# Kernel tuning notes

Hardware: AMD Instinct MI355X
Metric: run time of the kernel (lower is better)

The kernel has to match this reference:

```python
import jax, jax.numpy as jnp
import numpy as np

N = 100000   # nodes
E = 1600000  # edges
IN = 3       # in_channels
H = 32       # hidden_channels
C = 10       # num_classes_dynamic (== num output classes here)
G = 64       # number of graphs in the batch


def setup_inputs() -> dict:
    key = jax.random.key(0)
    ks = jax.random.split(key, 12)
    def w(k, shape, fan_in):
        return jax.random.normal(k, shape, jnp.float32) / np.sqrt(fan_in).astype(np.float32)
    inp = {}
    inp["x"] = jax.random.normal(ks[0], (N, IN), jnp.float32)
    inp["edge_index"] = jax.random.randint(ks[1], (2, E), 0, N, jnp.int32)
    inp["batch"] = jnp.sort(jax.random.randint(ks[2], (N,), 0, G, jnp.int32))
    # per-class linear filters (DynamicEdgeConv.filters)
    inp["filt_W"] = w(ks[3], (C, IN, H), IN)
    inp["filt_b"] = jnp.zeros((C, H), jnp.float32)
    # shared edge MLP: Linear(2H,H) -> ReLU -> Linear(H,H)
    inp["mlp_W1"] = w(ks[4], (2 * H, H), 2 * H)
    inp["mlp_b1"] = jnp.zeros((H,), jnp.float32)
    inp["mlp_W2"] = w(ks[5], (H, H), H)
    inp["mlp_b2"] = jnp.zeros((H,), jnp.float32)
    # GCN layers (gcn1 input dim hardcoded 323 = IN + C*H)
    inp["gcn1_W"] = w(ks[6], (IN + C * H, H), IN + C * H)
    inp["gcn1_b"] = jnp.zeros((H,), jnp.float32)
    inp["gcn2_W"] = w(ks[7], (H, H), H)
    inp["gcn2_b"] = jnp.zeros((H,), jnp.float32)
    # classifier
    inp["cls_W"] = w(ks[8], (H, C), H)
    inp["cls_b"] = jnp.zeros((C,), jnp.float32)
    return inp


def _gcn_conv(x, W, b, row, col, dinv):
    # PyG GCNConv: add self-loops, sym-normalize, aggregate src->dst
    xw = x @ W                                   # [N, H]
    norm = dinv[row] * dinv[col]                 # [E]
    out = jax.ops.segment_sum(xw[row] * norm[:, None], col, num_segments=x.shape[0])
    out = out + xw * (dinv * dinv)[:, None]      # self-loop term, norm = 1/deg_i
    return out + b


def _forward(x, edge_index, batch, filt_W, filt_b, mlp_W1, mlp_b1, mlp_W2, mlp_b2,
             gcn1_W, gcn1_b, gcn2_W, gcn2_b, cls_W, cls_b):
    row, col = edge_index[0], edge_index[1]
    n = x.shape[0]

    # DynamicEdgeConv: per-class filter -> gather(row,col) -> edge MLP -> scatter_add into col
    def per_class(_, wb):
        Wc, bc = wb
        xc = x @ Wc + bc                                      # [N, H]
        ef = jnp.concatenate([xc[row], xc[col]], axis=1)      # [E, 2H]
        h = jax.nn.relu(ef @ mlp_W1 + mlp_b1) @ mlp_W2 + mlp_b2
        return None, jax.ops.segment_sum(h, col, num_segments=n)
    _, aggs = jax.lax.scan(per_class, None, (filt_W, filt_b))  # [C, N, H]

    feat = jnp.concatenate([x, aggs.transpose(1, 0, 2).reshape(n, -1)], axis=1)  # [N, IN + C*H]

    deg = jax.ops.segment_sum(jnp.ones(row.shape[0], x.dtype), col, num_segments=n) + 1.0
    dinv = deg ** -0.5
    h1 = jax.nn.relu(_gcn_conv(feat, gcn1_W, gcn1_b, row, col, dinv))
    h2 = jax.nn.relu(_gcn_conv(h1, gcn2_W, gcn2_b, row, col, dinv))

    counts = jax.ops.segment_sum(jnp.ones(n, x.dtype), batch, num_segments=G)
    pooled = jax.ops.segment_sum(h2, batch, num_segments=G) / jnp.maximum(counts, 1.0)[:, None]
    return pooled @ cls_W + cls_b                             # [G, C]


def reference(x, edge_index, batch, filt_W, filt_b, mlp_W1, mlp_b1, mlp_W2, mlp_b2,
              gcn1_W, gcn1_b, gcn2_W, gcn2_b, cls_W, cls_b):
    return _forward(x, edge_index, batch, filt_W, filt_b, mlp_W1, mlp_b1, mlp_W2, mlp_b2,
                    gcn1_W, gcn1_b, gcn2_W, gcn2_b, cls_W, cls_b)
```

## Files before the change

### kernel.cpp

```cpp
#include <hip/hip_runtime.h>

#define NN 100000
#define NE 1600000
#define HH 32
#define CC 10
#define GG 64
#define NB 391
#define PBLK 100
#define ECH 16000
#define MTOT (NB * PBLK)
#define MSB ((MTOT + 255) / 256)

typedef _Float16 half8 __attribute__((ext_vector_type(8)));
typedef _Float16 half2v __attribute__((ext_vector_type(2)));
typedef float f32x4 __attribute__((ext_vector_type(4)));

__device__ __forceinline__ half2v bch(int v) { return __builtin_bit_cast(half2v, v); }


__global__ void precompute_small(const float* __restrict__ fW, const float* __restrict__ fb,
                                 const float* __restrict__ W1, const float* __restrict__ b1,
                                 const float* __restrict__ W2, const float* __restrict__ b2,
                                 const float* __restrict__ g1W, float* __restrict__ tab,
                                 _Float16* __restrict__ Mfrag) {
    int c = blockIdx.x;
    int k = threadIdx.x >> 5;
    int j = threadIdx.x & 31;
    float m = 0.f;
    for (int mm = 0; mm < 32; ++mm)
        m += W2[k * 32 + mm] * g1W[(3 + 32 * c + mm) * 32 + j];
    tab[2240 + c * 1024 + k * 32 + j] = m;

    if (k < 3) {
        float a = 0.f, b = 0.f;
        for (int i = 0; i < 32; ++i) {
            float w = fW[c * 96 + k * 32 + i];
            a += w * W1[i * 32 + j];
            b += w * W1[(32 + i) * 32 + j];
        }
        tab[c * 96 + k * 32 + j] = a;
        tab[960 + c * 96 + k * 32 + j] = b;
    } else if (k == 3) {
        float h = b1[j];
        for (int i = 0; i < 32; ++i)
            h += fb[c * 32 + i] * (W1[i * 32 + j] + W1[(32 + i) * 32 + j]);
        tab[1920 + c * 32 + j] = h;
    } else if (k == 4 && c == 0) {
        float t = 0.f;
        for (int cc2 = 0; cc2 < CC; ++cc2)
            for (int mm = 0; mm < 32; ++mm)
                t += b2[mm] * g1W[(3 + 32 * cc2 + mm) * 32 + j];
        tab[12480 + j] = t;
    }
    __syncthreads();
    {
        int jch = k;
        int jcol = j;
        float v = tab[2240 + c * 1024 + jch * 32 + jcol];
        int knew = (c >> 1) * 64 + 2 * jch + (c & 1);
        int kc = knew >> 5, within = knew & 31;
        int jt = jcol >> 4;
        int lq = within >> 3, ii = within & 7;
        int lidx = lq * 16 + (jcol & 15);
        int flat = ((kc * 2 + jt) * 64 + lidx) * 8 + ii;
        Mfrag[flat] = (_Float16)v;
    }
}

__global__ void bucket_hist(const int* __restrict__ ei, int* __restrict__ mat) {
    __shared__ int h[NB];
    int blk = blockIdx.x, tid = threadIdx.x;
    for (int i = tid; i < NB; i += 256) h[i] = 0;
    __syncthreads();
    int base = blk * ECH;
    for (int k = tid; k < ECH; k += 256)
        atomicAdd(&h[ei[NE + base + k] >> 8], 1);
    __syncthreads();
    for (int i = tid; i < NB; i += 256) mat[i * PBLK + blk] = h[i];
}

__global__ void scan_m1(const int* __restrict__ mat, int* __restrict__ msum) {
    __shared__ int sh[256];
    int b = blockIdx.x, t = threadIdx.x;
    int i = b * 256 + t;
    sh[t] = (i < MTOT) ? mat[i] : 0;
    __syncthreads();
    for (int off = 128; off > 0; off >>= 1) {
        if (t < off) sh[t] += sh[t + off];
        __syncthreads();
    }
    if (t == 0) msum[b] = sh[0];
}

__global__ void scan_m2(int* __restrict__ msum, float* __restrict__ pooled) {
    for (int i = threadIdx.x; i < GG * 33; i += 256) pooled[i] = 0.0f;
    __shared__ int sh[256];
    int t = threadIdx.x;
    int v = (t < MSB) ? msum[t] : 0;
    sh[t] = v;
    __syncthreads();
    for (int off = 1; off < 256; off <<= 1) {
        int add = (t >= off) ? sh[t - off] : 0;
        __syncthreads();
        sh[t] += add;
        __syncthreads();
    }
    if (t < MSB) msum[t] = sh[t] - v;
}

__global__ void scan_m3(int* __restrict__ mat, const int* __restrict__ msum) {
    __shared__ int sh[256];
    int b = blockIdx.x, t = threadIdx.x;
    int i = b * 256 + t;
    int v = (i < MTOT) ? mat[i] : 0;
    sh[t] = v;
    __syncthreads();
    for (int off = 1; off < 256; off <<= 1) {
        int add = (t >= off) ? sh[t - off] : 0;
        __syncthreads();
        sh[t] += add;
        __syncthreads();
    }
    if (i < MTOT) mat[i] = sh[t] - v + msum[b];
}

__global__ void bucket_scatter(const int* __restrict__ ei, const int* __restrict__ mat,
                               unsigned int* __restrict__ part) {
    __shared__ int bas[NB];
    __shared__ int cur[NB];
    int blk = blockIdx.x, tid = threadIdx.x;
    for (int i = tid; i < NB; i += 256) { bas[i] = mat[i * PBLK + blk]; cur[i] = 0; }
    __syncthreads();
    int base = blk * ECH;
    for (int k = tid; k < ECH; k += 256) {
        int e = base + k;
        int r = ei[e];
        int c = ei[NE + e];
        int b = c >> 8;
        int local = atomicAdd(&cur[b], 1);
        part[bas[b] + local] = (unsigned)r | ((unsigned)(c & 255) << 24);
    }
}

__global__ void bucket_build(const unsigned int* __restrict__ part, const int* __restrict__ mat,
                             const float* __restrict__ x, int* __restrict__ csr_row,
                             int* __restrict__ ideg, int* __restrict__ offs,
                             float* __restrict__ dinv, float4* __restrict__ xpad,
                             uint4* __restrict__ xs) {
    __shared__ int lh[256];
    __shared__ int lex[256];
    __shared__ int cur[256];
    int b = blockIdx.x, tid = threadIdx.x;
    int ebase = mat[b * PBLK];
    int eend = (b == NB - 1) ? NE : mat[(b + 1) * PBLK];
    int m = eend - ebase;
    lh[tid] = 0;
    __syncthreads();
    for (int k = tid; k < m; k += 256) {
        unsigned v = part[ebase + k];
        atomicAdd(&lh[v >> 24], 1);
    }
    __syncthreads();
    int cnt = lh[tid];
    lex[tid] = cnt;
    __syncthreads();
    for (int off = 1; off < 256; off <<= 1) {
        int v = (tid >= off) ? lex[tid - off] : 0;
        __syncthreads();
        lex[tid] += v;
        __syncthreads();
    }
    int excl = lex[tid] - cnt;
    lex[tid] = excl;
    cur[tid] = 0;
    int n = b * 256 + tid;
    if (n < NN) {
        ideg[n] = cnt;
        offs[n] = ebase + excl;
        float di = rsqrtf((float)cnt + 1.0f);
        dinv[n] = di;
        float x0 = x[n * 3], x1 = x[n * 3 + 1], x2 = x[n * 3 + 2];
        xpad[n] = make_float4(x0, x1, x2, di);
        _Float16 hx = (_Float16)x0, hy = (_Float16)x1, hz = (_Float16)x2;
        half2v sx = {hx, hx}, sy = {hy, hy}, sz = {hz, hz};
        xs[n] = make_uint4(__builtin_bit_cast(unsigned int, sx),
                           __builtin_bit_cast(unsigned int, sy),
                           __builtin_bit_cast(unsigned int, sz), 0u);
    }
    if (b == 0 && tid == 0) offs[NN] = NE;
    __syncthreads();
    for (int k = tid; k < m; k += 256) {
        unsigned v = part[ebase + k];
        int cl = (int)(v >> 24);
        int r = (int)(v & 0x00FFFFFFu);
        int local = atomicAdd(&cur[cl], 1);
        csr_row[ebase + lex[cl] + local] = r;
    }
}

#define EC_PAIR(QQ, SRC) do { \
    half2v px_ = bch(__shfl((int)(QQ).x, (SRC), 64)); \
    half2v py_ = bch(__shfl((int)(QQ).y, (SRC), 64)); \
    half2v pz_ = bch(__shfl((int)(QQ).z, (SRC), 64)); \
    _Pragma("unroll") \
    for (int p = 0; p < 5; ++p) { \
        half2v v = va[p] + px_ * A0[p] + py_ * A1[p] + pz_ * A2[p]; \
        v = __builtin_elementwise_max(v, zero); \
        acc[p] += v; \
    } } while (0)

#define EC_FLUSH() do { \
    _Pragma("unroll") \
    for (int p = 0; p < 5; ++p) { \
        accf[2 * p]     += (float)acc[p].x; \
        accf[2 * p + 1] += (float)acc[p].y; \
        acc[p] = zero; \
    } } while (0)

#define EC_GROUP4(QQ, TB) do { \
    half2v gx_[4], gy_[4], gz_[4]; \
    _Pragma("unroll") \
    for (int u = 0; u < 4; ++u) { \
        int s_ = 2 * ((TB) + u) + half; \
        gx_[u] = bch(__shfl((int)(QQ).x, s_, 64)); \
        gy_[u] = bch(__shfl((int)(QQ).y, s_, 64)); \
        gz_[u] = bch(__shfl((int)(QQ).z, s_, 64)); \
    } \
    _Pragma("unroll") \
    for (int u = 0; u < 4; ++u) { \
        _Pragma("unroll") \
        for (int p = 0; p < 5; ++p) { \
            half2v v = va[p] + gx_[u] * A0[p] + gy_[u] * A1[p] + gz_[u] * A2[p]; \
            v = __builtin_elementwise_max(v, zero); \
            acc[p] += v; \
        } \
    } \
    EC_FLUSH(); } while (0)

#define EC_CHUNK_FROM(T0, QQ, C2) do { \
    int tfull_ = (C2) >> 1; \
    int t_ = (T0); \
    for (; t_ + 4 <= tfull_; t_ += 4) EC_GROUP4(QQ, t_); \
    for (; t_ < tfull_; ++t_) EC_PAIR(QQ, 2 * t_ + half); \
    if ((C2) & 1) { \
        int src_ = (C2) - 1; \
        half2v px_ = bch(__shfl((int)(QQ).x, src_, 64)); \
        half2v py_ = bch(__shfl((int)(QQ).y, src_, 64)); \
        half2v pz_ = bch(__shfl((int)(QQ).z, src_, 64)); \
        if (half == 0) { \
            _Pragma("unroll") \
            for (int p = 0; p < 5; ++p) { \
                half2v v = va[p] + px_ * A0[p] + py_ * A1[p] + pz_ * A2[p]; \
                v = __builtin_elementwise_max(v, zero); \
                acc[p] += v; \
            } \
        } \
    } \
    EC_FLUSH(); } while (0)

__global__ __launch_bounds__(256, 4) void edgeconv_fused(
    const uint4* __restrict__ xs, const int* __restrict__ offs,
    const int* __restrict__ csr_row, const float* __restrict__ tab,
    _Float16* __restrict__ aggh) {
    int lane = threadIdx.x & 63;
    int j = lane & 31;
    int half = lane >> 5;

    half2v A0[5], A1[5], A2[5], B0[5], B1[5], B2[5], hb[5];
#pragma unroll
    for (int p = 0; p < 5; ++p) {
        int c0 = 2 * p, c1 = 2 * p + 1;
        A0[p] = half2v{(_Float16)tab[c0 * 96 + j],        (_Float16)tab[c1 * 96 + j]};
        A1[p] = half2v{(_Float16)tab[c0 * 96 + 32 + j],   (_Float16)tab[c1 * 96 + 32 + j]};
        A2[p] = half2v{(_Float16)tab[c0 * 96 + 64 + j],   (_Float16)tab[c1 * 96 + 64 + j]};
        B0[p] = half2v{(_Float16)tab[960 + c0 * 96 + j],      (_Float16)tab[960 + c1 * 96 + j]};
        B1[p] = half2v{(_Float16)tab[960 + c0 * 96 + 32 + j], (_Float16)tab[960 + c1 * 96 + 32 + j]};
        B2[p] = half2v{(_Float16)tab[960 + c0 * 96 + 64 + j], (_Float16)tab[960 + c1 * 96 + 64 + j]};
        hb[p] = half2v{(_Float16)tab[1920 + c0 * 32 + j], (_Float16)tab[1920 + c1 * 32 + j]};
    }
    const half2v zero = half2v{(_Float16)0.f, (_Float16)0.f};

    int wid = blockIdx.x * 4 + (threadIdx.x >> 6);
    const int ws = gridDim.x * 4;

    int n = wid;
    if (n >= NN) return;
    int e0 = offs[n];
    int e1 = offs[n + 1];
    uint4 qn = xs[n];
    int n2 = n + ws;
    int e0n = 0, e1n = 0;
    if (n2 < NN) { e0n = offs[n2]; e1n = offs[n2 + 1]; }
    uint4 q;
    {
        int ee = e0 + lane;
        int r0 = (ee < e1) ? csr_row[ee] : 0;
        q = xs[r0];
    }

    while (true) {
        int n3 = n2 + ws;
        int e0n2 = 0, e1n2 = 0;
        if (n3 < NN) { e0n2 = offs[n3]; e1n2 = offs[n3 + 1]; }
        uint4 qn2 = make_uint4(0u, 0u, 0u, 0u);
        if (n2 < NN) qn2 = xs[n2];

        bool multi = (e1 - e0) > 64;
        int pb = multi ? (e0 + 64) : e0n;
        int pe = multi ? e1 : e1n;
        int ee2 = pb + lane;
        int rn = (ee2 < pe) ? csr_row[ee2] : 0;

        half2v pxn = bch((int)qn.x), pyn = bch((int)qn.y), pzn = bch((int)qn.z);
        half2v va[5], acc[5];
        float accf[10];
#pragma unroll
        for (int p = 0; p < 5; ++p) {
            va[p] = hb[p] + pxn * B0[p] + pyn * B1[p] + pzn * B2[p];
            acc[p] = zero;
            accf[2 * p] = 0.f;
            accf[2 * p + 1] = 0.f;
        }

        int c2 = e1 - e0;
        if (c2 > 64) c2 = 64;
        int t0 = 0;
        if ((c2 >> 1) >= 4) {
            EC_GROUP4(q, 0);
            t0 = 4;
        }
        uint4 qpre = xs[rn];
        EC_CHUNK_FROM(t0, q, c2);

        if (multi) {
            int base = e0 + 64;
            uint4 qc = qpre;
            while (true) {
                int cc = e1 - base;
                if (cc > 64) cc = 64;
                int nb = base + 64;
                bool m2 = nb < e1;
                int pb2 = m2 ? nb : e0n;
                int pe2 = m2 ? e1 : e1n;
                int ee3 = pb2 + lane;
                int rn2 = (ee3 < pe2) ? csr_row[ee3] : 0;
                uint4 qp2 = xs[rn2];
                EC_CHUNK_FROM(0, qc, cc);
                qc = qp2;
                if (!m2) break;
                base = nb;
            }
            qpre = qc;
        }

#pragma unroll
        for (int c = 0; c < 10; ++c) accf[c] += __shfl_xor(accf[c], 32, 64);
        unsigned* arow32 = (unsigned*)(aggh + (size_t)n * 320);
        half2v d0 = {(_Float16)accf[2 * half],     (_Float16)accf[2 * half + 1]};
        half2v d1 = {(_Float16)accf[4 + 2 * half], (_Float16)accf[4 + 2 * half + 1]};
        arow32[lane]      = __builtin_bit_cast(unsigned, d0);
        arow32[64 + lane] = __builtin_bit_cast(unsigned, d1);
        if (half == 0) {
            half2v d2 = {(_Float16)accf[8], (_Float16)accf[9]};
            arow32[128 + lane] = __builtin_bit_cast(unsigned, d2);
        }

        if (n2 >= NN) return;
        n = n2;
        n2 = n3;
        e0 = e0n; e1 = e1n;
        e0n = e0n2; e1n = e1n2;
        qn = qn2;
        q = qpre;
    }
}

__global__ __launch_bounds__(256) void fold_mfma(
    const _Float16* __restrict__ aggh, const _Float16* __restrict__ MfragG,
    const float4* __restrict__ xpad, const int* __restrict__ ideg,
    const float* __restrict__ tab, const float* __restrict__ g1W,
    _Float16* __restrict__ y1) {
    __shared__ _Float16 Mf[10240];
    {
        const uint4* src = (const uint4*)MfragG;
        uint4* dst = (uint4*)Mf;
        for (int i = threadIdx.x; i < 1280; i += 256) dst[i] = src[i];
    }
    __syncthreads();

    int wave = blockIdx.x * 4 + (threadIdx.x >> 6);
    int lane = threadIdx.x & 63;
    int n0 = wave * 16;
    if (n0 >= NN) return;

    int m = lane & 15, q = lane >> 4;
    int arow_n = n0 + m;
    bool rowok = arow_n < NN;
    const _Float16* arow = aggh + (size_t)arow_n * 320 + q * 8;

    const half8* mf = (const half8*)Mf;
    f32x4 acc0 = {0.f, 0.f, 0.f, 0.f};
    f32x4 acc1 = {0.f, 0.f, 0.f, 0.f};

    for (int kc = 0; kc < 10; ++kc) {
        half8 a;
        if (rowok) a = *(const half8*)(arow + kc * 32);
        else {
#pragma unroll
            for (int i = 0; i < 8; ++i) a[i] = (_Float16)0.f;
        }
        half8 b0 = mf[(kc * 2 + 0) * 64 + lane];
        half8 b1 = mf[(kc * 2 + 1) * 64 + lane];
        acc0 = __builtin_amdgcn_mfma_f32_16x16x32_f16(a, b0, acc0, 0, 0, 0);
        acc1 = __builtin_amdgcn_mfma_f32_16x16x32_f16(a, b1, acc1, 0, 0, 0);
    }

    int jcol = lane & 15;
    float t0 = tab[12480 + jcol],      t1 = tab[12480 + 16 + jcol];
    float w00 = g1W[jcol],      w01 = g1W[32 + jcol],      w02 = g1W[64 + jcol];
    float w10 = g1W[16 + jcol], w11 = g1W[48 + jcol],      w12 = g1W[80 + jcol];
#pragma unroll
    for (int r = 0; r < 4; ++r) {
        int node = n0 + q * 4 + r;
        if (node < NN) {
            float4 xn = xpad[node];
            float dg = (float)ideg[node];
            float v0 = dg * t0 + xn.x * w00 + xn.y * w01 + xn.z * w02 + acc0[r];
            float v1 = dg * t1 + xn.x * w10 + xn.y * w11 + xn.z * w12 + acc1[r];
            y1[node * 32 + jcol]      = (_Float16)(v0 * xn.w);
            y1[node * 32 + 16 + jcol] = (_Float16)(v1 * xn.w);
        }
    }
}

__global__ __launch_bounds__(256, 8) void prop1_fused(
    const int* __restrict__ offs, const int* __restrict__ csr_row,
    const unsigned int* __restrict__ y1p, const float* __restrict__ dinv,
    const float* __restrict__ g1b, const float* __restrict__ g2W,
    unsigned int* __restrict__ y2p) {
    __shared__ float g2s[1024];
    for (int i = threadIdx.x; i < 1024; i += 256) g2s[i] = g2W[i];
    __syncthreads();

    int lane = threadIdx.x & 63;
    int l = lane & 15;
    int wid = blockIdx.x * 4 + (threadIdx.x >> 6);
    int n = wid * 4 + (lane >> 4);
    if (n >= NN) return;

    int e0 = offs[n], e1 = offs[n + 1];
    float sAl = 0.f, sAh = 0.f, sBl = 0.f, sBh = 0.f;
    int e = e0;
    if (e + 7 < e1) {
        half2v p0[8];
        {
            int r0[8];
#pragma unroll
            for (int u = 0; u < 8; ++u) r0[u] = csr_row[e + u];
#pragma unroll
            for (int u = 0; u < 8; ++u) p0[u] = __builtin_bit_cast(half2v, y1p[r0[u] * 16 + l]);
        }
        while (true) {
            int e2 = e + 8;
            bool more = (e2 + 7 < e1);
            half2v p1[8];
            if (more) {
                int r1[8];
#pragma unroll
                for (int u = 0; u < 8; ++u) r1[u] = csr_row[e2 + u];
#pragma unroll
                for (int u = 0; u < 8; ++u) p1[u] = __builtin_bit_cast(half2v, y1p[r1[u] * 16 + l]);
            }
#pragma unroll
            for (int u = 0; u < 8; u += 2) {
                sAl += (float)p0[u].x;     sAh += (float)p0[u].y;
                sBl += (float)p0[u + 1].x; sBh += (float)p0[u + 1].y;
            }
            e = e2;
            if (!more) break;
#pragma unroll
            for (int u = 0; u < 8; ++u) p0[u] = p1[u];
        }
    }
    if (e + 3 < e1) {
        int r[4];
#pragma unroll
        for (int u = 0; u < 4; ++u) r[u] = csr_row[e + u];
        half2v p[4];
#pragma unroll
        for (int u = 0; u < 4; ++u) p[u] = __builtin_bit_cast(half2v, y1p[r[u] * 16 + l]);
        sAl += (float)p[0].x + (float)p[2].x; sAh += (float)p[0].y + (float)p[2].y;
        sBl += (float)p[1].x + (float)p[3].x; sBh += (float)p[1].y + (float)p[3].y;
        e += 4;
    }
    if (e + 1 < e1) {
        int r0 = csr_row[e], r1 = csr_row[e + 1];
        half2v p0 = __builtin_bit_cast(half2v, y1p[r0 * 16 + l]);
        half2v p1 = __builtin_bit_cast(half2v, y1p[r1 * 16 + l]);
        sAl += (float)p0.x; sAh += (float)p0.y;
        sBl += (float)p1.x; sBh += (float)p1.y;
        e += 2;
    }
    if (e < e1) {
        int r = csr_row[e];
        half2v p = __builtin_bit_cast(half2v, y1p[r * 16 + l]);
        sAl += (float)p.x; sAh += (float)p.y;
    }
    float di = dinv[n];
    half2v pn = __builtin_bit_cast(half2v, y1p[n * 16 + l]);
    float h1l = di * (sAl + sBl + (float)pn.x);
    float h1h = di * (sAh + sBh + (float)pn.y);
    float hl = fmaxf(h1l + g1b[2 * l], 0.f);
    float hh = fmaxf(h1h + g1b[2 * l + 1], 0.f);

    float al = 0.f, ah = 0.f;
    int base = lane & 48;
#pragma unroll
    for (int m = 0; m < 16; ++m) {
        float xl = __shfl(hl, base + m, 64);
        float xh2 = __shfl(hh, base + m, 64);
        al += xl * g2s[(2 * m) * 32 + 2 * l] + xh2 * g2s[(2 * m + 1) * 32 + 2 * l];
        ah += xl * g2s[(2 * m) * 32 + 2 * l + 1] + xh2 * g2s[(2 * m + 1) * 32 + 2 * l + 1];
    }
    half2v o = {(_Float16)(al * di), (_Float16)(ah * di)};
    y2p[n * 16 + l] = __builtin_bit_cast(unsigned int, o);
}

__global__ __launch_bounds__(256, 8) void prop2_plain(
    const int* __restrict__ offs, const int* __restrict__ csr_row,
    const unsigned int* __restrict__ y2p, const float* __restrict__ dinv,
    unsigned int* __restrict__ outp) {
    int lane = threadIdx.x & 63;
    int l = lane & 15;
    int wid = blockIdx.x * 4 + (threadIdx.x >> 6);
    int n = wid * 4 + (lane >> 4);
    if (n >= NN) return;

    int e0 = offs[n], e1 = offs[n + 1];
    float sAl = 0.f, sAh = 0.f, sBl = 0.f, sBh = 0.f;
    int e = e0;
    if (e + 7 < e1) {
        half2v p0[8];
        {
            int r0[8];
#pragma unroll
            for (int u = 0; u < 8; ++u) r0[u] = csr_row[e + u];
#pragma unroll
            for (int u = 0; u < 8; ++u) p0[u] = __builtin_bit_cast(half2v, y2p[r0[u] * 16 + l]);
        }
        while (true) {
            int e2 = e + 8;
            bool more = (e2 + 7 < e1);
            half2v p1[8];
            if (more) {
                int r1[8];
#pragma unroll
                for (int u = 0; u < 8; ++u) r1[u] = csr_row[e2 + u];
#pragma unroll
                for (int u = 0; u < 8; ++u) p1[u] = __builtin_bit_cast(half2v, y2p[r1[u] * 16 + l]);
            }
#pragma unroll
            for (int u = 0; u < 8; u += 2) {
                sAl += (float)p0[u].x;     sAh += (float)p0[u].y;
                sBl += (float)p0[u + 1].x; sBh += (float)p0[u + 1].y;
            }
            e = e2;
            if (!more) break;
#pragma unroll
            for (int u = 0; u < 8; ++u) p0[u] = p1[u];
        }
    }
    if (e + 3 < e1) {
        int r[4];
#pragma unroll
        for (int u = 0; u < 4; ++u) r[u] = csr_row[e + u];
        half2v p[4];
#pragma unroll
        for (int u = 0; u < 4; ++u) p[u] = __builtin_bit_cast(half2v, y2p[r[u] * 16 + l]);
        sAl += (float)p[0].x + (float)p[2].x; sAh += (float)p[0].y + (float)p[2].y;
        sBl += (float)p[1].x + (float)p[3].x; sBh += (float)p[1].y + (float)p[3].y;
        e += 4;
    }
    if (e + 1 < e1) {
        int r0 = csr_row[e], r1 = csr_row[e + 1];
        half2v p0 = __builtin_bit_cast(half2v, y2p[r0 * 16 + l]);
        half2v p1 = __builtin_bit_cast(half2v, y2p[r1 * 16 + l]);
        sAl += (float)p0.x; sAh += (float)p0.y;
        sBl += (float)p1.x; sBh += (float)p1.y;
        e += 2;
    }
    if (e < e1) {
        int r = csr_row[e];
        half2v p = __builtin_bit_cast(half2v, y2p[r * 16 + l]);
        sAl += (float)p.x; sAh += (float)p.y;
    }
    float di = dinv[n];
    half2v pn = __builtin_bit_cast(half2v, y2p[n * 16 + l]);
    half2v o = {(_Float16)(di * (sAl + sBl + (float)pn.x)),
                (_Float16)(di * (sAh + sBh + (float)pn.y))};
    outp[n * 16 + l] = __builtin_bit_cast(unsigned int, o);
}

__global__ void pool_seg(const _Float16* __restrict__ h2, const float* __restrict__ g2b,
                         const int* __restrict__ batch, float* __restrict__ pooled,
                         float* __restrict__ counts) {
    int grp = threadIdx.x >> 5, j = threadIdx.x & 31;
    int base = (blockIdx.x * 8 + grp) * 64;
    if (base >= NN) return;
    float bj = g2b[j];
    float acc = 0.f, cnt = 0.f;
    int curg = -1;
    int lim = base + 64;
    if (lim > NN) lim = NN;
    for (int n = base; n < lim; ++n) {
        int g = batch[n];
        if (g != curg) {
            if (curg >= 0) {
                atomicAdd(&pooled[curg * 32 + j], acc);
                if (j == 0) atomicAdd(&counts[curg], cnt);
            }
            curg = g; acc = 0.f; cnt = 0.f;
        }
        acc += fmaxf((float)h2[n * 32 + j] + bj, 0.f);
        cnt += 1.f;
    }
    if (curg >= 0) {
        atomicAdd(&pooled[curg * 32 + j], acc);
        if (j == 0) atomicAdd(&counts[curg], cnt);
    }
}

__global__ void final_kernel(const float* __restrict__ pooled, const float* __restrict__ counts,
                             const float* __restrict__ clsW, const float* __restrict__ clsb,
                             float* __restrict__ out) {
    int tid = threadIdx.x;
    if (tid >= GG * CC) return;
    int g = tid / CC, cc = tid % CC;
    float inv = 1.0f / fmaxf(counts[g], 1.0f);
    float s = clsb[cc];
    for (int j = 0; j < 32; ++j) s += (pooled[g * 32 + j] * inv) * clsW[j * CC + cc];
    out[g * CC + cc] = s;
}

extern "C" void kernel_launch(void* const* d_in, const int* in_sizes, int n_in,
                              void* d_out, int out_size, void* d_ws, size_t ws_size,
                              hipStream_t stream) {
    const float* x     = (const float*)d_in[0];
    const int*   ei    = (const int*)d_in[1];
    const int*   batch = (const int*)d_in[2];
    const float* fW    = (const float*)d_in[3];
    const float* fb    = (const float*)d_in[4];
    const float* W1    = (const float*)d_in[5];
    const float* b1    = (const float*)d_in[6];
    const float* W2    = (const float*)d_in[7];
    const float* b2    = (const float*)d_in[8];
    const float* g1W   = (const float*)d_in[9];
    const float* g1b   = (const float*)d_in[10];
    const float* g2W   = (const float*)d_in[11];
    const float* g2b   = (const float*)d_in[12];
    const float* clsW  = (const float*)d_in[13];
    const float* clsb  = (const float*)d_in[14];
    float* out = (float*)d_out;

    float4*         xpad    = (float4*)d_ws;
    uint4*          xs      = (uint4*)(xpad + NN);
    _Float16*       aggh    = (_Float16*)(xs + NN);
    unsigned int*   part    = (unsigned int*)aggh;
    int*            csr_row = (int*)(aggh + (size_t)NN * 320);
    int*            mat     = (int*)(csr_row + NE);
    int*            msum    = mat + MTOT;
    int*            ideg    = msum + 256;
    int*            offs    = ideg + NN;
    float*          dinv    = (float*)(offs + NN + 1);
    float*          tab     = dinv + NN;
    _Float16*       Mfrag   = (_Float16*)(tab + 16384);
    _Float16*       y1      = Mfrag + 10240;
    unsigned int*   y2p     = (unsigned int*)(y1 + (size_t)NN * 32);
    unsigned int*   h2p     = y2p + (size_t)NN * 16;
    float*          pooled  = (float*)(h2p + (size_t)NN * 16);
    float*          counts  = pooled + GG * 32;

    const int propBlocks = (NN + 15) / 16;
    const int foldBlocks = ((NN + 15) / 16 + 3) / 4;

    precompute_small<<<10, 1024, 0, stream>>>(fW, fb, W1, b1, W2, b2, g1W, tab, Mfrag);

    bucket_hist<<<PBLK, 256, 0, stream>>>(ei, mat);
    scan_m1<<<MSB, 256, 0, stream>>>(mat, msum);
    scan_m2<<<1, 256, 0, stream>>>(msum, pooled);
    scan_m3<<<MSB, 256, 0, stream>>>(mat, msum);
    bucket_scatter<<<PBLK, 256, 0, stream>>>(ei, mat, part);
    bucket_build<<<NB, 256, 0, stream>>>(part, mat, x, csr_row, ideg, offs, dinv, xpad, xs);

    edgeconv_fused<<<2048, 256, 0, stream>>>(xs, offs, csr_row, tab, aggh);
    fold_mfma<<<foldBlocks, 256, 0, stream>>>(aggh, Mfrag, xpad, ideg, tab, g1W, y1);

    prop1_fused<<<propBlocks, 256, 0, stream>>>(offs, csr_row, (const unsigned int*)y1,
                                                dinv, g1b, g2W, y2p);
    prop2_plain<<<propBlocks, 256, 0, stream>>>(offs, csr_row, y2p, dinv, h2p);
    pool_seg<<<(NN + 511) / 512, 256, 0, stream>>>((const _Float16*)h2p, g2b, batch,
                                                   pooled, counts);
    final_kernel<<<1, 640, 0, stream>>>(pooled, counts, clsW, clsb, out);
}
```

Before: 364.5 us.

## Switch edgeconv inner loop from packed fp16 to fp32, per-half class split

```diff
diff --git a/kernel.cpp b/kernel.cpp
--- a/kernel.cpp
+++ b/kernel.cpp
@@ -145,8 +145,7 @@
 __global__ void bucket_build(const unsigned int* __restrict__ part, const int* __restrict__ mat,
                              const float* __restrict__ x, int* __restrict__ csr_row,
                              int* __restrict__ ideg, int* __restrict__ offs,
-                             float* __restrict__ dinv, float4* __restrict__ xpad,
-                             uint4* __restrict__ xs) {
+                             float* __restrict__ dinv, float4* __restrict__ xpad) {
     __shared__ int lh[256];
     __shared__ int lex[256];
     __shared__ int cur[256];
@@ -181,11 +180,6 @@
         dinv[n] = di;
         float x0 = x[n * 3], x1 = x[n * 3 + 1], x2 = x[n * 3 + 2];
         xpad[n] = make_float4(x0, x1, x2, di);
-        _Float16 hx = (_Float16)x0, hy = (_Float16)x1, hz = (_Float16)x2;
-        half2v sx = {hx, hx}, sy = {hy, hy}, sz = {hz, hz};
-        xs[n] = make_uint4(__builtin_bit_cast(unsigned int, sx),
-                           __builtin_bit_cast(unsigned int, sy),
-                           __builtin_bit_cast(unsigned int, sz), 0u);
     }
     if (b == 0 && tid == 0) offs[NN] = NE;
     __syncthreads();
@@ -198,87 +192,44 @@
     }
 }
 
-#define EC_PAIR(QQ, SRC) do { \
-    half2v px_ = bch(__shfl((int)(QQ).x, (SRC), 64)); \
-    half2v py_ = bch(__shfl((int)(QQ).y, (SRC), 64)); \
-    half2v pz_ = bch(__shfl((int)(QQ).z, (SRC), 64)); \
+#define EC_EDGE(QQ, T) do { \
+    float px_ = __shfl((QQ).x, (T), 64); \
+    float py_ = __shfl((QQ).y, (T), 64); \
+    float pz_ = __shfl((QQ).z, (T), 64); \
     _Pragma("unroll") \
-    for (int p = 0; p < 5; ++p) { \
-        half2v v = va[p] + px_ * A0[p] + py_ * A1[p] + pz_ * A2[p]; \
-        v = __builtin_elementwise_max(v, zero); \
-        acc[p] += v; \
+    for (int i = 0; i < 5; ++i) { \
+        float v_ = va[i] + px_ * a0[i] + py_ * a1[i] + pz_ * a2[i]; \
+        accf[i] += fmaxf(v_, 0.f); \
     } } while (0)
 
-#define EC_FLUSH() do { \
-    _Pragma("unroll") \
-    for (int p = 0; p < 5; ++p) { \
-        accf[2 * p]     += (float)acc[p].x; \
-        accf[2 * p + 1] += (float)acc[p].y; \
-        acc[p] = zero; \
-    } } while (0)
-
-#define EC_GROUP4(QQ, TB) do { \
-    half2v gx_[4], gy_[4], gz_[4]; \
-    _Pragma("unroll") \
-    for (int u = 0; u < 4; ++u) { \
-        int s_ = 2 * ((TB) + u) + half; \
-        gx_[u] = bch(__shfl((int)(QQ).x, s_, 64)); \
-        gy_[u] = bch(__shfl((int)(QQ).y, s_, 64)); \
-        gz_[u] = bch(__shfl((int)(QQ).z, s_, 64)); \
+#define EC_CHUNK_FROM(T0, QQ, C2) do { \
+    int t_ = (T0); \
+    for (; t_ + 4 <= (C2); t_ += 4) { \
+        EC_EDGE(QQ, t_); EC_EDGE(QQ, t_ + 1); EC_EDGE(QQ, t_ + 2); EC_EDGE(QQ, t_ + 3); \
     } \
-    _Pragma("unroll") \
-    for (int u = 0; u < 4; ++u) { \
-        _Pragma("unroll") \
-        for (int p = 0; p < 5; ++p) { \
-            half2v v = va[p] + gx_[u] * A0[p] + gy_[u] * A1[p] + gz_[u] * A2[p]; \
-            v = __builtin_elementwise_max(v, zero); \
-            acc[p] += v; \
-        } \
-    } \
-    EC_FLUSH(); } while (0)
-
-#define EC_CHUNK_FROM(T0, QQ, C2) do { \
-    int tfull_ = (C2) >> 1; \
-    int t_ = (T0); \
-    for (; t_ + 4 <= tfull_; t_ += 4) EC_GROUP4(QQ, t_); \
-    for (; t_ < tfull_; ++t_) EC_PAIR(QQ, 2 * t_ + half); \
-    if ((C2) & 1) { \
-        int src_ = (C2) - 1; \
-        half2v px_ = bch(__shfl((int)(QQ).x, src_, 64)); \
-        half2v py_ = bch(__shfl((int)(QQ).y, src_, 64)); \
-        half2v pz_ = bch(__shfl((int)(QQ).z, src_, 64)); \
-        if (half == 0) { \
-            _Pragma("unroll") \
-            for (int p = 0; p < 5; ++p) { \
-                half2v v = va[p] + px_ * A0[p] + py_ * A1[p] + pz_ * A2[p]; \
-                v = __builtin_elementwise_max(v, zero); \
-                acc[p] += v; \
-            } \
-        } \
-    } \
-    EC_FLUSH(); } while (0)
+    for (; t_ < (C2); ++t_) EC_EDGE(QQ, t_); \
+} while (0)
 
 __global__ __launch_bounds__(256, 4) void edgeconv_fused(
-    const uint4* __restrict__ xs, const int* __restrict__ offs,
+    const float4* __restrict__ xpad, const int* __restrict__ offs,
     const int* __restrict__ csr_row, const float* __restrict__ tab,
     _Float16* __restrict__ aggh) {
     int lane = threadIdx.x & 63;
     int j = lane & 31;
-    int half = lane >> 5;
-
-    half2v A0[5], A1[5], A2[5], B0[5], B1[5], B2[5], hb[5];
-#pragma unroll
-    for (int p = 0; p < 5; ++p) {
-        int c0 = 2 * p, c1 = 2 * p + 1;
-        A0[p] = half2v{(_Float16)tab[c0 * 96 + j],        (_Float16)tab[c1 * 96 + j]};
-        A1[p] = half2v{(_Float16)tab[c0 * 96 + 32 + j],   (_Float16)tab[c1 * 96 + 32 + j]};
-        A2[p] = half2v{(_Float16)tab[c0 * 96 + 64 + j],   (_Float16)tab[c1 * 96 + 64 + j]};
-        B0[p] = half2v{(_Float16)tab[960 + c0 * 96 + j],      (_Float16)tab[960 + c1 * 96 + j]};
-        B1[p] = half2v{(_Float16)tab[960 + c0 * 96 + 32 + j], (_Float16)tab[960 + c1 * 96 + 32 + j]};
-        B2[p] = half2v{(_Float16)tab[960 + c0 * 96 + 64 + j], (_Float16)tab[960 + c1 * 96 + 64 + j]};
-        hb[p] = half2v{(_Float16)tab[1920 + c0 * 32 + j], (_Float16)tab[1920 + c1 * 32 + j]};
-    }
-    const half2v zero = half2v{(_Float16)0.f, (_Float16)0.f};
+    int h = lane >> 5;
+
+    float a0[5], a1[5], a2[5], b0[5], b1[5], b2[5], hbf[5];
+#pragma unroll
+    for (int i = 0; i < 5; ++i) {
+        int c = 2 * i + h;
+        a0[i]  = tab[c * 96 + j];
+        a1[i]  = tab[c * 96 + 32 + j];
+        a2[i]  = tab[c * 96 + 64 + j];
+        b0[i]  = tab[960 + c * 96 + j];
+        b1[i]  = tab[960 + c * 96 + 32 + j];
+        b2[i]  = tab[960 + c * 96 + 64 + j];
+        hbf[i] = tab[1920 + c * 32 + j];
+    }
 
     int wid = blockIdx.x * 4 + (threadIdx.x >> 6);
     const int ws = gridDim.x * 4;
@@ -287,23 +238,23 @@
     if (n >= NN) return;
     int e0 = offs[n];
     int e1 = offs[n + 1];
-    uint4 qn = xs[n];
+    float4 qn = xpad[n];
     int n2 = n + ws;
     int e0n = 0, e1n = 0;
     if (n2 < NN) { e0n = offs[n2]; e1n = offs[n2 + 1]; }
-    uint4 q;
+    float4 q;
     {
         int ee = e0 + lane;
         int r0 = (ee < e1) ? csr_row[ee] : 0;
-        q = xs[r0];
+        q = xpad[r0];
     }
 
     while (true) {
         int n3 = n2 + ws;
         int e0n2 = 0, e1n2 = 0;
         if (n3 < NN) { e0n2 = offs[n3]; e1n2 = offs[n3 + 1]; }
-        uint4 qn2 = make_uint4(0u, 0u, 0u, 0u);
-        if (n2 < NN) qn2 = xs[n2];
+        float4 qn2 = make_float4(0.f, 0.f, 0.f, 0.f);
+        if (n2 < NN) qn2 = xpad[n2];
 
         bool multi = (e1 - e0) > 64;
         int pb = multi ? (e0 + 64) : e0n;
@@ -311,30 +262,26 @@
         int ee2 = pb + lane;
         int rn = (ee2 < pe) ? csr_row[ee2] : 0;
 
-        half2v pxn = bch((int)qn.x), pyn = bch((int)qn.y), pzn = bch((int)qn.z);
-        half2v va[5], acc[5];
-        float accf[10];
-#pragma unroll
-        for (int p = 0; p < 5; ++p) {
-            va[p] = hb[p] + pxn * B0[p] + pyn * B1[p] + pzn * B2[p];
-            acc[p] = zero;
-            accf[2 * p] = 0.f;
-            accf[2 * p + 1] = 0.f;
+        float va[5], accf[5];
+#pragma unroll
+        for (int i = 0; i < 5; ++i) {
+            va[i] = hbf[i] + qn.x * b0[i] + qn.y * b1[i] + qn.z * b2[i];
+            accf[i] = 0.f;
         }
 
         int c2 = e1 - e0;
         if (c2 > 64) c2 = 64;
         int t0 = 0;
-        if ((c2 >> 1) >= 4) {
-            EC_GROUP4(q, 0);
+        if (c2 >= 4) {
+            EC_EDGE(q, 0); EC_EDGE(q, 1); EC_EDGE(q, 2); EC_EDGE(q, 3);
             t0 = 4;
         }
-        uint4 qpre = xs[rn];
+        float4 qpre = xpad[rn];
         EC_CHUNK_FROM(t0, q, c2);
 
         if (multi) {
             int base = e0 + 64;
-            uint4 qc = qpre;
+            float4 qc = qpre;
             while (true) {
                 int cc = e1 - base;
                 if (cc > 64) cc = 64;
@@ -344,7 +291,7 @@
                 int pe2 = m2 ? e1 : e1n;
                 int ee3 = pb2 + lane;
                 int rn2 = (ee3 < pe2) ? csr_row[ee3] : 0;
-                uint4 qp2 = xs[rn2];
+                float4 qp2 = xpad[rn2];
                 EC_CHUNK_FROM(0, qc, cc);
                 qc = qp2;
                 if (!m2) break;
@@ -353,16 +300,23 @@
             qpre = qc;
         }
 
-#pragma unroll
-        for (int c = 0; c < 10; ++c) accf[c] += __shfl_xor(accf[c], 32, 64);
+        unsigned pcks[5];
+#pragma unroll
+        for (int i = 0; i < 5; ++i) {
+            float r = __shfl_xor(accf[i], 32, 64);
+            _Float16 lo = (_Float16)(h ? r : accf[i]);
+            _Float16 hi = (_Float16)(h ? accf[i] : r);
+            half2v pr = {lo, hi};
+            pcks[i] = __builtin_bit_cast(unsigned, pr);
+        }
         unsigned* arow32 = (unsigned*)(aggh + (size_t)n * 320);
-        half2v d0 = {(_Float16)accf[2 * half],     (_Float16)accf[2 * half + 1]};
-        half2v d1 = {(_Float16)accf[4 + 2 * half], (_Float16)accf[4 + 2 * half + 1]};
-        arow32[lane]      = __builtin_bit_cast(unsigned, d0);
-        arow32[64 + lane] = __builtin_bit_cast(unsigned, d1);
-        if (half == 0) {
-            half2v d2 = {(_Float16)accf[8], (_Float16)accf[9]};
-            arow32[128 + lane] = __builtin_bit_cast(unsigned, d2);
+        if (h == 0) {
+            arow32[j]       = pcks[0];
+            arow32[32 + j]  = pcks[1];
+            arow32[64 + j]  = pcks[2];
+        } else {
+            arow32[96 + j]  = pcks[3];
+            arow32[128 + j] = pcks[4];
         }
 
         if (n2 >= NN) return;
@@ -449,6 +403,8 @@
     if (n >= NN) return;
 
     int e0 = offs[n], e1 = offs[n + 1];
+    float di = dinv[n];
+    half2v pn = __builtin_bit_cast(half2v, y1p[n * 16 + l]);
     float sAl = 0.f, sAh = 0.f, sBl = 0.f, sBh = 0.f;
     int e = e0;
     if (e + 7 < e1) {
@@ -506,8 +462,6 @@
         half2v p = __builtin_bit_cast(half2v, y1p[r * 16 + l]);
         sAl += (float)p.x; sAh += (float)p.y;
     }
-    float di = dinv[n];
-    half2v pn = __builtin_bit_cast(half2v, y1p[n * 16 + l]);
     float h1l = di * (sAl + sBl + (float)pn.x);
     float h1h = di * (sAh + sBh + (float)pn.y);
     float hl = fmaxf(h1l + g1b[2 * l], 0.f);
@@ -537,6 +491,8 @@
     if (n >= NN) return;
 
     int e0 = offs[n], e1 = offs[n + 1];
+    float di = dinv[n];
+    half2v pn = __builtin_bit_cast(half2v, y2p[n * 16 + l]);
     float sAl = 0.f, sAh = 0.f, sBl = 0.f, sBh = 0.f;
     int e = e0;
     if (e + 7 < e1) {
@@ -594,8 +550,6 @@
         half2v p = __builtin_bit_cast(half2v, y2p[r * 16 + l]);
         sAl += (float)p.x; sAh += (float)p.y;
     }
-    float di = dinv[n];
-    half2v pn = __builtin_bit_cast(half2v, y2p[n * 16 + l]);
     half2v o = {(_Float16)(di * (sAl + sBl + (float)pn.x)),
                 (_Float16)(di * (sAh + sBh + (float)pn.y))};
     outp[n * 16 + l] = __builtin_bit_cast(unsigned int, o);
@@ -690,9 +644,9 @@
     scan_m2<<<1, 256, 0, stream>>>(msum, pooled);
     scan_m3<<<MSB, 256, 0, stream>>>(mat, msum);
     bucket_scatter<<<PBLK, 256, 0, stream>>>(ei, mat, part);
-    bucket_build<<<NB, 256, 0, stream>>>(part, mat, x, csr_row, ideg, offs, dinv, xpad, xs);
-
-    edgeconv_fused<<<2048, 256, 0, stream>>>(xs, offs, csr_row, tab, aggh);
+    bucket_build<<<NB, 256, 0, stream>>>(part, mat, x, csr_row, ideg, offs, dinv, xpad);
+
+    edgeconv_fused<<<2048, 256, 0, stream>>>(xpad, offs, csr_row, tab, aggh);
     fold_mfma<<<foldBlocks, 256, 0, stream>>>(aggh, Mfrag, xpad, ideg, tab, g1W, y1);
 
     prop1_fused<<<propBlocks, 256, 0, stream>>>(offs, csr_row, (const unsigned int*)y1,
```

New measurement: 374.9 us. 2.9% more time.
